# Kernel optimization log

Measured on AMD Instinct MI355X. Metric: run time of the kernel, lower is better.

The kernel has to match this reference:

```python
import jax, jax.numpy as jnp
from jax import lax
import numpy as np

NUM_HEAD = 4
D_MODEL = 160
HEAD_DIM = D_MODEL // NUM_HEAD  # 40
FEAT_DIM = 64
F_SIZE = (128, 128)
B = 4
LN_EPS = 1e-5
LEAKY_SLOPE = 0.01
DN = ('NCHW', 'OIHW', 'NCHW')


def setup_inputs() -> dict:
    key = jax.random.key(0)
    ks = jax.random.split(key, 10)
    pe_len = (F_SIZE[0] // 2) * (F_SIZE[1] // 2) + 1  # 4097
    s = 0.05
    return {
        'x': jax.random.normal(ks[0], (B, FEAT_DIM, F_SIZE[0], F_SIZE[1]), jnp.float32),
        'conv1_w': jax.random.normal(ks[1], (FEAT_DIM, FEAT_DIM, 2, 2), jnp.float32) * s,
        'conv1_b': jax.random.normal(ks[2], (FEAT_DIM,), jnp.float32) * s,
        'conv2_w': jax.random.normal(ks[3], (D_MODEL, FEAT_DIM, 1, 1), jnp.float32) * s,
        'conv2_b': jax.random.normal(ks[4], (D_MODEL,), jnp.float32) * s,
        'pe': jax.random.uniform(ks[5], (pe_len, 1), jnp.float32),
        'wq': jax.random.normal(ks[6], (D_MODEL, D_MODEL), jnp.float32) * s,
        'wk': jax.random.normal(ks[7], (D_MODEL, D_MODEL), jnp.float32) * s,
        'wv': jax.random.normal(ks[8], (D_MODEL, D_MODEL), jnp.float32) * s,
        'ln_w': jnp.ones((D_MODEL,), jnp.float32),
        'ln_b': jnp.zeros((D_MODEL,), jnp.float32),
    }


def reference(x, conv1_w, conv1_b, conv2_w, conv2_b, pe, wq, wk, wv, ln_w, ln_b):
    b = x.shape[0]
    # patch embed: stride-2 conv -> 1x1 conv -> LeakyReLU
    f = lax.conv_general_dilated(x, conv1_w, (2, 2), 'VALID', dimension_numbers=DN)
    f = f + conv1_b[None, :, None, None]
    f = lax.conv_general_dilated(f, conv2_w, (1, 1), 'VALID', dimension_numbers=DN)
    f = f + conv2_b[None, :, None, None]
    f = jnp.where(f >= 0, f, LEAKY_SLOPE * f)
    _, c, h, w = f.shape  # [b, 160, 64, 64]
    f = f.reshape(b, c, h * w).transpose(0, 2, 1)  # [b, s, d]
    # pad one extra token at end of sequence, add positional encoding [s+1, 1]
    f = jnp.pad(f, ((0, 0), (0, 1), (0, 0))) + pe  # [b, s+1, d]
    s1 = f.shape[1]
    # torch Linear (no bias): y = x @ W.T
    q = (f @ wq.T).reshape(b, s1, NUM_HEAD, HEAD_DIM).transpose(0, 2, 1, 3)
    k = (f @ wk.T).reshape(b, s1, NUM_HEAD, HEAD_DIM).transpose(0, 2, 1, 3)
    v = (f @ wv.T).reshape(b, s1, NUM_HEAD, HEAD_DIM).transpose(0, 2, 1, 3)
    score = jnp.einsum('bhqd,bhkd->bhqk', q, k) / jnp.sqrt(jnp.float32(HEAD_DIM))
    score = jax.nn.softmax(score, axis=-1)
    att = jnp.einsum('bhqk,bhkd->bhqd', score, v)  # [b, h, s+1, hd]
    cat = att.transpose(0, 2, 1, 3).reshape(b, s1, D_MODEL)
    feat = cat[:, :-1, :]  # drop padded token -> [b, s, d]
    # residual LayerNorm: LN(feat) + feat
    mu = jnp.mean(feat, axis=-1, keepdims=True)
    var = jnp.mean(jnp.square(feat - mu), axis=-1, keepdims=True)
    ln = (feat - mu) / jnp.sqrt(var + LN_EPS) * ln_w + ln_b
    feat = ln + feat
    feat = feat.transpose(0, 2, 1).reshape(b, D_MODEL, h, w)  # [b, 160, 64, 64]
    feat = jnp.repeat(jnp.repeat(feat, 2, axis=2), 2, axis=3)
    return feat
```

## Files before the change

kernel.cpp:

```cpp
#include <hip/hip_runtime.h>

typedef _Float16 f16;
typedef _Float16 half2v __attribute__((ext_vector_type(2)));
typedef _Float16 half4v __attribute__((ext_vector_type(4)));
typedef _Float16 half8 __attribute__((ext_vector_type(8)));
typedef float f32x4 __attribute__((ext_vector_type(4)));
typedef unsigned u32x4 __attribute__((ext_vector_type(4)));

#define MFMA16(a, b, c) __builtin_amdgcn_mfma_f32_16x16x32_f16((a), (b), (c), 0, 0, 0)

__device__ __forceinline__ unsigned pk2(float a, float b) {
  return __builtin_bit_cast(unsigned, __builtin_amdgcn_cvt_pkrtz(a, b));
}

__device__ __forceinline__ void plswap_pair(unsigned& a, unsigned& b) {
  asm("s_nop 1\n\t"
      "v_permlane32_swap_b32 %0, %1\n\t"
      "v_permlane16_swap_b32 %0, %1"
      : "+v"(a), "+v"(b));
}


__global__ __launch_bounds__(256) void k_prep(
    const float* __restrict__ wq, const float* __restrict__ wk,
    const float* __restrict__ wv, f16* __restrict__ wf) {
  int kind = blockIdx.y;
  const float* src = (kind == 0) ? wq : (kind == 1 ? wk : wv);
  int i4 = blockIdx.x * 256 + threadIdx.x;
  f32x4 v = *(const f32x4*)(src + i4 * 4);
  uint2 u = {pk2(v[0], v[1]), pk2(v[2], v[3])};
  *(uint2*)(wf + (size_t)kind * 25600 + i4 * 4) = u;
}

__global__ __launch_bounds__(256) void k_conv(
    const float* __restrict__ x, const float* __restrict__ w1, const float* __restrict__ b1,
    const float* __restrict__ w2, const float* __restrict__ b2, const float* __restrict__ pe,
    const float* __restrict__ wq, const float* __restrict__ wk, const float* __restrict__ wv,
    f16* __restrict__ fh, f16* __restrict__ q_h, f16* __restrict__ k_h,
    f16* __restrict__ vt_h, float* __restrict__ kmaxp) {
  __shared__ __attribute__((aligned(16))) char smem[112192];
  f16* fT   = (f16*)smem;
  f16* xh   = (f16*)(smem + 21504);
  f16* w1h  = (f16*)(smem + 55360);
  f16* c1t  = (f16*)(smem + 55360);
  float* red160 = (float*)(smem + 64576);
  f16* w2h  = (f16*)(smem + 89152);

  const float c1l = 0.15811388300841898f * 1.4426950408889634f;

  int y = blockIdx.x, b = blockIdx.y;
  int t = threadIdx.x, lane = t & 63, wv4 = t >> 6, quad = lane >> 4, col = lane & 15;
  int s0 = y * 64;

  const float* xb = x + (b * 64) * 16384 + (2 * y) * 128;
#pragma unroll
  for (int it = 0; it < 32; ++it) {
    int flat = t + it * 256;
    int pos = flat & 63, r = (flat >> 6) & 1, ci = flat >> 7;
    float2 v = *(const float2*)(xb + ci * 16384 + r * 128 + 2 * pos);
    *(unsigned*)(xh + pos * 264 + ci * 4 + r * 2) = pk2(v.x, v.y);
  }
#pragma unroll
  for (int it = 0; it < 16; ++it) {
    int i4 = t + it * 256;
    int co = i4 >> 6, q4 = (i4 & 63) * 4;
    f32x4 v = *(const f32x4*)(w1 + co * 256 + q4);
    uint2 u = {pk2(v[0], v[1]), pk2(v[2], v[3])};
    *(uint2*)(w1h + co * 264 + q4) = u;
  }
#pragma unroll
  for (int it = 0; it < 10; ++it) {
    int i4 = t + it * 256;
    int c2 = i4 >> 4, q4 = (i4 & 15) * 4;
    f32x4 v = *(const f32x4*)(w2 + c2 * 64 + q4);
    uint2 u = {pk2(v[0], v[1]), pk2(v[2], v[3])};
    *(uint2*)(w2h + c2 * 72 + q4) = u;
  }
  __syncthreads();

  float b1v[4];
#pragma unroll
  for (int r = 0; r < 4; ++r) b1v[r] = b1[wv4 * 16 + quad * 4 + r];
  f32x4 acc1[4];
#pragma unroll
  for (int nt = 0; nt < 4; ++nt)
#pragma unroll
    for (int r = 0; r < 4; ++r) acc1[nt][r] = b1v[r];
#pragma unroll
  for (int kk = 0; kk < 8; ++kk) {
    half8 a = *(half8*)(w1h + (wv4 * 16 + col) * 264 + kk * 32 + quad * 8);
#pragma unroll
    for (int nt = 0; nt < 4; ++nt) {
      half8 bfr = *(half8*)(xh + (nt * 16 + col) * 264 + kk * 32 + quad * 8);
      acc1[nt] = MFMA16(a, bfr, acc1[nt]);
    }
  }
  __syncthreads();
#pragma unroll
  for (int nt = 0; nt < 4; ++nt) {
    uint2 u = {pk2(acc1[nt][0], acc1[nt][1]), pk2(acc1[nt][2], acc1[nt][3])};
    *(uint2*)(c1t + (nt * 16 + col) * 72 + wv4 * 16 + quad * 4) = u;
  }
  __syncthreads();

  f32x4 acc2[10];
#pragma unroll
  for (int mt = 0; mt < 10; ++mt)
#pragma unroll
    for (int r = 0; r < 4; ++r) acc2[mt][r] = b2[mt * 16 + quad * 4 + r];
  half8 bb0 = *(half8*)(c1t + (wv4 * 16 + col) * 72 + quad * 8);
  half8 bb1 = *(half8*)(c1t + (wv4 * 16 + col) * 72 + 32 + quad * 8);
#pragma unroll
  for (int mt = 0; mt < 10; ++mt) {
    half8 a0 = *(half8*)(w2h + (mt * 16 + col) * 72 + quad * 8);
    half8 a1 = *(half8*)(w2h + (mt * 16 + col) * 72 + 32 + quad * 8);
    acc2[mt] = MFMA16(a0, bb0, acc2[mt]);
    acc2[mt] = MFMA16(a1, bb1, acc2[mt]);
  }
  float pes = pe[s0 + wv4 * 16 + col];
#pragma unroll
  for (int mt = 0; mt < 10; ++mt) {
    float p[4];
#pragma unroll
    for (int r = 0; r < 4; ++r) {
      float v = acc2[mt][r];
      v = (v >= 0.f) ? v : 0.01f * v;
      p[r] = v + pes;
    }
    uint2 u = {pk2(p[0], p[1]), pk2(p[2], p[3])};
    *(uint2*)(fT + (wv4 * 16 + col) * 168 + mt * 16 + quad * 4) = u;
  }
  __syncthreads();

#pragma unroll
  for (int it = 0; it < 5; ++it) {
    int flat = t + it * 256;
    int row = flat / 20, seg = flat - row * 20;
    *(uint4*)(fh + ((size_t)b * 4096 + s0 + row) * 160 + seg * 8) =
        *(const uint4*)(fT + row * 168 + seg * 8);
  }

  if (y == 63) {
    float pe4 = pe[4096];
    if (t < 160) {
      int hh = t / 40, d = t - hh * 40, bh = b * 4 + hh;
#pragma unroll
      for (int kind = 0; kind < 3; ++kind) {
        const float* wsp = (kind == 0) ? wq : (kind == 1 ? wk : wv);
        const float* wr = wsp + t * 160;
        float rs = 0.f;
#pragma unroll
        for (int c4 = 0; c4 < 40; ++c4) {
          f32x4 v = *(const f32x4*)(wr + c4 * 4);
          rs += v[0] + v[1] + v[2] + v[3];
        }
        float val = pe4 * rs;
        if (kind == 0)      q_h[((size_t)bh * 4097 + 4096) * 40 + d] = (f16)(val * c1l);
        else if (kind == 1) { k_h[((size_t)bh * 4160 + 4096) * 40 + d] = (f16)val;
                              red160[t] = val * val; }
        else                vt_h[((size_t)bh * 40 + d) * 4160 + 4096] = (f16)val;
      }
    }
    __syncthreads();
    if (t < 4) {
      float s = 0.f;
#pragma unroll
      for (int j = 0; j < 40; ++j) s += red160[t * 40 + j];
      kmaxp[(b * 4 + t) * 65 + 64] = s;
    }
  }
}

__global__ __launch_bounds__(256) void k_qkv(
    const f16* __restrict__ fh, const f16* __restrict__ wf,
    f16* __restrict__ q_h, f16* __restrict__ k_h, f16* __restrict__ vt_h) {
  __shared__ __attribute__((aligned(16))) f16 Lv[160 * 72];
  int y = blockIdx.x, b = blockIdx.y, kind = blockIdx.z;
  int t = threadIdx.x, lane = t & 63, wvv = t >> 6, quad = lane >> 4, col = lane & 15;
  int s0 = y * 64;
  const float c1l = 0.15811388300841898f * 1.4426950408889634f;
  const f16* wk_ = wf + (size_t)kind * 25600;

  half8 af[5];
  int rowA = wvv * 16 + col;
#pragma unroll
  for (int kk = 0; kk < 5; ++kk)
    af[kk] = *(const half8*)(fh + ((size_t)b * 4096 + s0 + rowA) * 160 + kk * 32 + quad * 8);

#pragma unroll
  for (int n0 = 0; n0 < 10; ++n0) {
    f32x4 acc; acc[0] = 0.f; acc[1] = 0.f; acc[2] = 0.f; acc[3] = 0.f;
    int rowB = n0 * 16 + col;
#pragma unroll
    for (int kk = 0; kk < 5; ++kk) {
      half8 bf = *(const half8*)(wk_ + rowB * 160 + kk * 32 + quad * 8);
      acc = MFMA16(af[kk], bf, acc);
    }
    int o = n0 * 16 + col;
    int hh = o / 40, d = o - hh * 40;
    int bh = b * 4 + hh;
    if (kind == 2) {
      half4v hv;
#pragma unroll
      for (int r = 0; r < 4; ++r) hv[r] = (f16)acc[r];
      *(half4v*)(Lv + o * 72 + wvv * 16 + quad * 4) = hv;
    } else {
#pragma unroll
      for (int r = 0; r < 4; ++r) {
        int s = s0 + wvv * 16 + quad * 4 + r;
        if (kind == 0) q_h[((size_t)bh * 4097 + s) * 40 + d] = (f16)(acc[r] * c1l);
        else           k_h[((size_t)bh * 4160 + s) * 40 + d] = (f16)acc[r];
      }
    }
  }
  if (kind == 2) {
    __syncthreads();
#pragma unroll
    for (int it = 0; it < 5; ++it) {
      int c = t + it * 256;
      int row = c >> 3, seg = c & 7;
      int hh = row / 40, d = row - hh * 40;
      *(uint4*)(vt_h + ((size_t)(b * 4 + hh) * 40 + d) * 4160 + s0 + seg * 8) =
          *(const uint4*)(Lv + row * 72 + seg * 8);
    }
  }
}

__global__ __launch_bounds__(256) void k_sq(
    const f16* __restrict__ k_h, float* __restrict__ kmaxp) {
  int t = threadIdx.x, lane = t & 63, wvv = t >> 6;
  int slot = blockIdx.x * 4 + wvv;
  int bh = blockIdx.y;
  int s = slot * 64 + lane;
  const f16* kr = k_h + ((size_t)bh * 4160 + s) * 40;
  float sum = 0.f;
#pragma unroll
  for (int i = 0; i < 5; ++i) {
    half8 v = *(const half8*)(kr + i * 8);
#pragma unroll
    for (int j = 0; j < 8; ++j) { float xv = (float)v[j]; sum += xv * xv; }
  }
#pragma unroll
  for (int d = 1; d < 64; d <<= 1) sum = fmaxf(sum, __shfl_xor(sum, d));
  if (lane == 0) kmaxp[bh * 65 + slot] = sum;
}

__global__ __launch_bounds__(256, 4) void k_attn(
    const f16* __restrict__ q_h, const f16* __restrict__ k_h,
    const f16* __restrict__ vt_h, const float* __restrict__ kmaxp,
    float* __restrict__ pacc) {
  __shared__ __attribute__((aligned(16))) f16 Ks[2][64 * 40];
  __shared__ __attribute__((aligned(16))) f16 Vs[2][40 * 72];
  __shared__ __attribute__((aligned(16))) f16 Ones[8];
  __shared__ __attribute__((aligned(16))) f16 Zro[8];
  __shared__ __attribute__((aligned(16))) float red4[4];

  int qt = blockIdx.x, bh = blockIdx.y, ks = blockIdx.z;
  int qbase = qt * 128;
  int t = threadIdx.x, lane = t & 63, wv = t >> 6, quad = lane >> 4, col = lane & 15;
  int gbase = ks * 33;
  int nIter = 33 - ks;

  if (t < 8) { Zro[t] = (f16)0; Ones[t] = (f16)1; }
  {
    float vm = (t < 65) ? kmaxp[bh * 65 + t] : 0.f;
#pragma unroll
    for (int d = 1; d < 64; d <<= 1) vm = fmaxf(vm, __shfl_xor(vm, d));
    if (lane == 0) red4[wv] = vm;
  }

  const f16* khb = k_h + ((size_t)bh * 4160 + gbase * 64) * 40;
  const f16* vtb = vt_h + (size_t)bh * 40 * 4160;
  int vrow = t >> 3, vseg = t & 7;
  uint4 rka = *(const uint4*)(khb + t * 8);
  uint4 rkb = {0, 0, 0, 0}, rvb = {0, 0, 0, 0};
  if (t < 64) rkb = *(const uint4*)(khb + (256 + t) * 8);
  uint4 rva = *(const uint4*)(vtb + vrow * 4160 + gbase * 64 + vseg * 8);
  if (t < 64) rvb = *(const uint4*)(vtb + (32 + vrow) * 4160 + gbase * 64 + vseg * 8);

  half8 zero8;
#pragma unroll
  for (int j = 0; j < 8; ++j) zero8[j] = (f16)0;

  half8 bq[2][2], q32[2];
#pragma unroll
  for (int nt = 0; nt < 2; ++nt) {
    const f16* qr = q_h + ((size_t)bh * 4097 + qbase + wv * 32 + nt * 16 + col) * 40;
    bq[nt][0] = *(const half8*)(qr + quad * 8);
    q32[nt] = *(const half8*)(qr + 32);
  }
  __syncthreads();

  float mk = fmaxf(fmaxf(red4[0], red4[1]), fmaxf(red4[2], red4[3]));

#pragma unroll
  for (int nt = 0; nt < 2; ++nt) {
    float s = 0.f;
#pragma unroll
    for (int j = 0; j < 8; ++j) {
      float a0 = (float)bq[nt][0][j];
      s += a0 * a0;
    }
    s += __shfl_xor(s, 16);
    s += __shfl_xor(s, 32);
#pragma unroll
    for (int j = 0; j < 8; ++j) {
      float a1 = (float)q32[nt][j];
      s += a1 * a1;
    }
    float mfl = sqrtf(s * mk) - 14.0f;
    half8 e = zero8;
    e[0] = (f16)(-mfl);
    bq[nt][1] = (quad == 0) ? q32[nt] : ((quad == 1) ? e : zero8);
  }

  f32x4 o_[2][3];
#pragma unroll
  for (int a = 0; a < 2; ++a)
#pragma unroll
    for (int b2 = 0; b2 < 3; ++b2)
#pragma unroll
      for (int r = 0; r < 4; ++r) o_[a][b2][r] = 0.f;

  for (int kt = 0; kt < nIter; ++kt) {
    int bsel = kt & 1;
    int g = gbase + kt;
    *(uint4*)(&Ks[bsel][t * 8]) = rka;
    if (t < 64) *(uint4*)(&Ks[bsel][(256 + t) * 8]) = rkb;
    *(uint4*)(&Vs[bsel][vrow * 72 + vseg * 8]) = rva;
    if (t < 64) *(uint4*)(&Vs[bsel][(32 + vrow) * 72 + vseg * 8]) = rvb;
    if (kt + 1 < nIter) {
      const f16* kn = khb + (size_t)(kt + 1) * 2560;
      int k0n = (g + 1) << 6;
      rka = *(const uint4*)(kn + t * 8);
      if (t < 64) rkb = *(const uint4*)(kn + (256 + t) * 8);
      rva = *(const uint4*)(vtb + vrow * 4160 + k0n + vseg * 8);
      if (t < 64) rvb = *(const uint4*)(vtb + (32 + vrow) * 4160 + k0n + vseg * 8);
    }
    __syncthreads();

    bool lastt = (g == 64);

    f32x4 acc[4][2];
#pragma unroll
    for (int mt = 0; mt < 4; ++mt) {
      int row = mt * 16 + col;
      half8 ak0 = *(half8*)(&Ks[bsel][row * 40 + quad * 8]);
      const f16* pa1 = (quad == 0) ? &Ks[bsel][row * 40 + 32]
                                   : ((quad == 1) ? Ones : Zro);
      half8 ak1 = *(half8*)pa1;
#pragma unroll
      for (int nt = 0; nt < 2; ++nt) {
        f32x4 a; a[0] = 0.f; a[1] = 0.f; a[2] = 0.f; a[3] = 0.f;
        a = MFMA16(ak0, bq[nt][0], a);
        a = MFMA16(ak1, bq[nt][1], a);
        acc[mt][nt] = a;
      }
    }

    half8 pa[2][2];
#pragma unroll
    for (int kk2 = 0; kk2 < 2; ++kk2)
#pragma unroll
      for (int nt = 0; nt < 2; ++nt) {
        float p0[4], p1[4];
#pragma unroll
        for (int r = 0; r < 4; ++r) {
          p0[r] = __builtin_amdgcn_exp2f(acc[kk2 * 2][nt][r]);
          p1[r] = __builtin_amdgcn_exp2f(acc[kk2 * 2 + 1][nt][r]);
        }
        if (__builtin_expect(lastt, 0)) {
#pragma unroll
          for (int r = 0; r < 4; ++r) {
            p0[r] = (kk2 == 0 && (quad * 4 + r) == 0) ? p0[r] : 0.f;
            p1[r] = 0.f;
          }
        }
        unsigned sr[4];
        sr[0] = pk2(p0[0], p0[1]);
        sr[1] = pk2(p0[2], p0[3]);
        sr[2] = pk2(p1[0], p1[1]);
        sr[3] = pk2(p1[2], p1[3]);
        plswap_pair(sr[0], sr[2]);
        plswap_pair(sr[1], sr[3]);
        u32x4 uu; uu[0] = sr[0]; uu[1] = sr[1]; uu[2] = sr[2]; uu[3] = sr[3];
        pa[kk2][nt] = __builtin_bit_cast(half8, uu);
      }

#pragma unroll
    for (int kk2 = 0; kk2 < 2; ++kk2)
#pragma unroll
      for (int nv = 0; nv < 3; ++nv) {
        int d = nv * 16 + col;
        const f16* vp = (d < 40) ? &Vs[bsel][d * 72 + kk2 * 32 + quad * 8]
                                 : ((d == 40) ? Ones : Zro);
        half8 bv = *(half8*)vp;
        o_[0][nv] = MFMA16(pa[kk2][0], bv, o_[0][nv]);
        o_[1][nv] = MFMA16(pa[kk2][1], bv, o_[1][nv]);
      }
  }

  float* pb = pacc + (size_t)(ks * 16 + bh) * 4096 * 48;
#pragma unroll
  for (int mtq = 0; mtq < 2; ++mtq)
#pragma unroll
    for (int nv = 0; nv < 3; ++nv)
#pragma unroll
      for (int r = 0; r < 4; ++r) {
        int q = qbase + wv * 32 + mtq * 16 + quad * 4 + r;
        pb[(size_t)q * 48 + nv * 16 + col] = o_[mtq][nv][r];
      }
}

__global__ __launch_bounds__(256) void k_ln_out(
    const float* __restrict__ pacc, const float* __restrict__ lnw,
    const float* __restrict__ lnb, float* __restrict__ out) {
  __shared__ float g[16 * 164];
  __shared__ float linv[16 * 4];
  int y = blockIdx.x, b = blockIdx.y, z = blockIdx.z, t = threadIdx.x;
  const size_t P1 = (size_t)16 * 4096 * 48;
  int w0 = z * 16;
  if (t < 64) {
    int row = t >> 2, h = t & 3;
    size_t i0 = ((size_t)(b * 4 + h) * 4096 + y * 64 + w0 + row) * 48 + 40;
    linv[row * 4 + h] = 1.f / (pacc[i0] + pacc[P1 + i0]);
  }
  __syncthreads();
#pragma unroll
  for (int it = 0; it < 3; ++it) {
    int flat = t + it * 256;
    if (flat < 640) {
      int row = flat / 40, dq = flat - row * 40;
      int h = dq / 10, d = (dq - h * 10) * 4;
      size_t idx = ((size_t)(b * 4 + h) * 4096 + y * 64 + w0 + row) * 48 + d;
      f32x4 v0 = *(const f32x4*)(pacc + idx);
      f32x4 v1 = *(const f32x4*)(pacc + P1 + idx);
      float li = linv[row * 4 + h];
      f32x4 gv;
#pragma unroll
      for (int j = 0; j < 4; ++j) gv[j] = (v0[j] + v1[j]) * li;
      *(f32x4*)(g + row * 164 + h * 40 + d) = gv;
    }
  }
  __syncthreads();
  int row = t >> 4, part = t & 15;
  float* gr = g + row * 164 + part * 10;
  float s1 = 0.f, s2 = 0.f;
#pragma unroll
  for (int j = 0; j < 10; ++j) { float v = gr[j]; s1 += v; s2 += v * v; }
  s1 += __shfl_xor(s1, 1); s1 += __shfl_xor(s1, 2);
  s1 += __shfl_xor(s1, 4); s1 += __shfl_xor(s1, 8);
  s2 += __shfl_xor(s2, 1); s2 += __shfl_xor(s2, 2);
  s2 += __shfl_xor(s2, 4); s2 += __shfl_xor(s2, 8);
  float mu = s1 * (1.f / 160.f);
  float var = s2 * (1.f / 160.f) - mu * mu;
  float inv = rsqrtf(var + 1e-5f);
  const float* lw = lnw + part * 10;
  const float* lb = lnb + part * 10;
#pragma unroll
  for (int j = 0; j < 10; ++j) {
    float v = gr[j];
    gr[j] = (v - mu) * inv * lw[j] + lb[j] + v;
  }
  __syncthreads();
  int Yo = t >> 7, rem = t & 127, xp = rem & 31, cpar = rem >> 5;
  int rl = xp >> 1;
  float* ob = out + (2 * y + Yo) * 128 + z * 32 + xp;
  for (int c = cpar; c < 160; c += 4)
    ob[(size_t)(b * 160 + c) * 16384] = g[rl * 164 + c];
}

extern "C" void kernel_launch(void* const* d_in, const int* in_sizes, int n_in,
                              void* d_out, int out_size, void* d_ws, size_t ws_size,
                              hipStream_t stream) {
  const float* x   = (const float*)d_in[0];
  const float* w1  = (const float*)d_in[1];
  const float* b1  = (const float*)d_in[2];
  const float* w2  = (const float*)d_in[3];
  const float* b2  = (const float*)d_in[4];
  const float* pe  = (const float*)d_in[5];
  const float* wq  = (const float*)d_in[6];
  const float* wk  = (const float*)d_in[7];
  const float* wvp = (const float*)d_in[8];
  const float* lnw = (const float*)d_in[9];
  const float* lnb = (const float*)d_in[10];
  float* out = (float*)d_out;

  char* p = (char*)d_ws;
  f16* q_h   = (f16*)p;   p += (size_t)16 * 4097 * 40 * 2;
  f16* k_h   = (f16*)p;   p += (size_t)16 * 4160 * 40 * 2;
  f16* vt_h  = (f16*)p;   p += (size_t)16 * 40 * 4160 * 2;
  float* pacc = (float*)p; p += (size_t)2 * 16 * 4096 * 48 * 4;
  float* kmaxp = (float*)p; p += 16 * 65 * 4;
  f16* fh    = (f16*)p;   p += (size_t)4 * 4096 * 160 * 2;
  f16* wf    = (f16*)p;   p += (size_t)3 * 160 * 160 * 2;

  k_prep<<<dim3(25, 3), 256, 0, stream>>>(wq, wk, wvp, wf);
  k_conv<<<dim3(64, 4), 256, 0, stream>>>(x, w1, b1, w2, b2, pe, wq, wk, wvp,
                                          fh, q_h, k_h, vt_h, kmaxp);
  k_qkv<<<dim3(64, 4, 3), 256, 0, stream>>>(fh, wf, q_h, k_h, vt_h);
  k_sq<<<dim3(16, 16), 256, 0, stream>>>(k_h, kmaxp);
  k_attn<<<dim3(32, 16, 2), 256, 0, stream>>>(q_h, k_h, vt_h, kmaxp, pacc);
  k_ln_out<<<dim3(64, 4, 4), 256, 0, stream>>>(pacc, lnw, lnb, out);
}
```

Measured before the change: 201.5 us.

## Split attention block into 8 waves with 16 queries each

After: 211.3 us. +4.8%, slower.

```diff
diff --git a/kernel.cpp b/kernel.cpp
--- a/kernel.cpp
+++ b/kernel.cpp
@@ -245,7 +245,7 @@
   if (lane == 0) kmaxp[bh * 65 + slot] = sum;
 }
 
-__global__ __launch_bounds__(256, 4) void k_attn(
+__global__ __launch_bounds__(512, 6) void k_attn(
     const f16* __restrict__ q_h, const f16* __restrict__ k_h,
     const f16* __restrict__ vt_h, const float* __restrict__ kmaxp,
     float* __restrict__ pacc) {
@@ -253,11 +253,11 @@
   __shared__ __attribute__((aligned(16))) f16 Vs[2][40 * 72];
   __shared__ __attribute__((aligned(16))) f16 Ones[8];
   __shared__ __attribute__((aligned(16))) f16 Zro[8];
-  __shared__ __attribute__((aligned(16))) float red4[4];
+  __shared__ __attribute__((aligned(16))) float red8[8];
 
   int qt = blockIdx.x, bh = blockIdx.y, ks = blockIdx.z;
   int qbase = qt * 128;
-  int t = threadIdx.x, lane = t & 63, wv = t >> 6, quad = lane >> 4, col = lane & 15;
+  int t = threadIdx.x, lane = t & 63, wid = t >> 6, quad = lane >> 4, col = lane & 15;
   int gbase = ks * 33;
   int nIter = 33 - ks;
 
@@ -266,82 +266,100 @@
     float vm = (t < 65) ? kmaxp[bh * 65 + t] : 0.f;
 #pragma unroll
     for (int d = 1; d < 64; d <<= 1) vm = fmaxf(vm, __shfl_xor(vm, d));
-    if (lane == 0) red4[wv] = vm;
+    if (lane == 0) red8[wid] = vm;
   }
 
   const f16* khb = k_h + ((size_t)bh * 4160 + gbase * 64) * 40;
   const f16* vtb = vt_h + (size_t)bh * 40 * 4160;
-  int vrow = t >> 3, vseg = t & 7;
-  uint4 rka = *(const uint4*)(khb + t * 8);
-  uint4 rkb = {0, 0, 0, 0}, rvb = {0, 0, 0, 0};
-  if (t < 64) rkb = *(const uint4*)(khb + (256 + t) * 8);
-  uint4 rva = *(const uint4*)(vtb + vrow * 4160 + gbase * 64 + vseg * 8);
-  if (t < 64) rvb = *(const uint4*)(vtb + (32 + vrow) * 4160 + gbase * 64 + vseg * 8);
+
+  uint4 r0, r1 = {0, 0, 0, 0};
+  {
+    int k00 = gbase << 6;
+    if (t < 320) {
+      r0 = *(const uint4*)(khb + t * 8);
+    } else {
+      int j = t - 320;
+      r0 = *(const uint4*)(vtb + (size_t)(j >> 3) * 4160 + k00 + (j & 7) * 8);
+    }
+    if (t < 128) {
+      int j = 192 + t;
+      r1 = *(const uint4*)(vtb + (size_t)(j >> 3) * 4160 + k00 + (j & 7) * 8);
+    }
+  }
 
   half8 zero8;
 #pragma unroll
   for (int j = 0; j < 8; ++j) zero8[j] = (f16)0;
 
-  half8 bq[2][2], q32[2];
-#pragma unroll
-  for (int nt = 0; nt < 2; ++nt) {
-    const f16* qr = q_h + ((size_t)bh * 4097 + qbase + wv * 32 + nt * 16 + col) * 40;
-    bq[nt][0] = *(const half8*)(qr + quad * 8);
-    q32[nt] = *(const half8*)(qr + 32);
-  }
-  __syncthreads();
-
-  float mk = fmaxf(fmaxf(red4[0], red4[1]), fmaxf(red4[2], red4[3]));
-
-#pragma unroll
-  for (int nt = 0; nt < 2; ++nt) {
+  half8 bq0, bq1, q32v;
+  {
+    const f16* qr = q_h + ((size_t)bh * 4097 + qbase + wid * 16 + col) * 40;
+    bq0 = *(const half8*)(qr + quad * 8);
+    q32v = *(const half8*)(qr + 32);
+  }
+  __syncthreads();
+
+  float mk = fmaxf(fmaxf(fmaxf(red8[0], red8[1]), fmaxf(red8[2], red8[3])),
+                   fmaxf(fmaxf(red8[4], red8[5]), fmaxf(red8[6], red8[7])));
+
+  {
     float s = 0.f;
 #pragma unroll
     for (int j = 0; j < 8; ++j) {
-      float a0 = (float)bq[nt][0][j];
+      float a0 = (float)bq0[j];
       s += a0 * a0;
     }
     s += __shfl_xor(s, 16);
     s += __shfl_xor(s, 32);
 #pragma unroll
     for (int j = 0; j < 8; ++j) {
-      float a1 = (float)q32[nt][j];
+      float a1 = (float)q32v[j];
       s += a1 * a1;
     }
     float mfl = sqrtf(s * mk) - 14.0f;
     half8 e = zero8;
     e[0] = (f16)(-mfl);
-    bq[nt][1] = (quad == 0) ? q32[nt] : ((quad == 1) ? e : zero8);
-  }
-
-  f32x4 o_[2][3];
-#pragma unroll
-  for (int a = 0; a < 2; ++a)
-#pragma unroll
-    for (int b2 = 0; b2 < 3; ++b2)
-#pragma unroll
-      for (int r = 0; r < 4; ++r) o_[a][b2][r] = 0.f;
+    bq1 = (quad == 0) ? q32v : ((quad == 1) ? e : zero8);
+  }
+
+  f32x4 o_[3];
+#pragma unroll
+  for (int nv = 0; nv < 3; ++nv)
+#pragma unroll
+    for (int r = 0; r < 4; ++r) o_[nv][r] = 0.f;
 
   for (int kt = 0; kt < nIter; ++kt) {
     int bsel = kt & 1;
     int g = gbase + kt;
-    *(uint4*)(&Ks[bsel][t * 8]) = rka;
-    if (t < 64) *(uint4*)(&Ks[bsel][(256 + t) * 8]) = rkb;
-    *(uint4*)(&Vs[bsel][vrow * 72 + vseg * 8]) = rva;
-    if (t < 64) *(uint4*)(&Vs[bsel][(32 + vrow) * 72 + vseg * 8]) = rvb;
+    if (t < 320) {
+      *(uint4*)(&Ks[bsel][t * 8]) = r0;
+    } else {
+      int j = t - 320;
+      *(uint4*)(&Vs[bsel][(j >> 3) * 72 + (j & 7) * 8]) = r0;
+    }
+    if (t < 128) {
+      int j = 192 + t;
+      *(uint4*)(&Vs[bsel][(j >> 3) * 72 + (j & 7) * 8]) = r1;
+    }
     if (kt + 1 < nIter) {
       const f16* kn = khb + (size_t)(kt + 1) * 2560;
       int k0n = (g + 1) << 6;
-      rka = *(const uint4*)(kn + t * 8);
-      if (t < 64) rkb = *(const uint4*)(kn + (256 + t) * 8);
-      rva = *(const uint4*)(vtb + vrow * 4160 + k0n + vseg * 8);
-      if (t < 64) rvb = *(const uint4*)(vtb + (32 + vrow) * 4160 + k0n + vseg * 8);
+      if (t < 320) {
+        r0 = *(const uint4*)(kn + t * 8);
+      } else {
+        int j = t - 320;
+        r0 = *(const uint4*)(vtb + (size_t)(j >> 3) * 4160 + k0n + (j & 7) * 8);
+      }
+      if (t < 128) {
+        int j = 192 + t;
+        r1 = *(const uint4*)(vtb + (size_t)(j >> 3) * 4160 + k0n + (j & 7) * 8);
+      }
     }
     __syncthreads();
 
     bool lastt = (g == 64);
 
-    f32x4 acc[4][2];
+    f32x4 acc[4];
 #pragma unroll
     for (int mt = 0; mt < 4; ++mt) {
       int row = mt * 16 + col;
@@ -349,43 +367,38 @@
       const f16* pa1 = (quad == 0) ? &Ks[bsel][row * 40 + 32]
                                    : ((quad == 1) ? Ones : Zro);
       half8 ak1 = *(half8*)pa1;
-#pragma unroll
-      for (int nt = 0; nt < 2; ++nt) {
-        f32x4 a; a[0] = 0.f; a[1] = 0.f; a[2] = 0.f; a[3] = 0.f;
-        a = MFMA16(ak0, bq[nt][0], a);
-        a = MFMA16(ak1, bq[nt][1], a);
-        acc[mt][nt] = a;
-      }
-    }
-
-    half8 pa[2][2];
-#pragma unroll
-    for (int kk2 = 0; kk2 < 2; ++kk2)
-#pragma unroll
-      for (int nt = 0; nt < 2; ++nt) {
-        float p0[4], p1[4];
+      f32x4 a; a[0] = 0.f; a[1] = 0.f; a[2] = 0.f; a[3] = 0.f;
+      a = MFMA16(ak0, bq0, a);
+      a = MFMA16(ak1, bq1, a);
+      acc[mt] = a;
+    }
+
+    half8 pa[2];
+#pragma unroll
+    for (int kk2 = 0; kk2 < 2; ++kk2) {
+      float p0[4], p1[4];
+#pragma unroll
+      for (int r = 0; r < 4; ++r) {
+        p0[r] = __builtin_amdgcn_exp2f(acc[kk2 * 2][r]);
+        p1[r] = __builtin_amdgcn_exp2f(acc[kk2 * 2 + 1][r]);
+      }
+      if (__builtin_expect(lastt, 0)) {
 #pragma unroll
         for (int r = 0; r < 4; ++r) {
-          p0[r] = __builtin_amdgcn_exp2f(acc[kk2 * 2][nt][r]);
-          p1[r] = __builtin_amdgcn_exp2f(acc[kk2 * 2 + 1][nt][r]);
+          p0[r] = (kk2 == 0 && (quad * 4 + r) == 0) ? p0[r] : 0.f;
+          p1[r] = 0.f;
         }
-        if (__builtin_expect(lastt, 0)) {
-#pragma unroll
-          for (int r = 0; r < 4; ++r) {
-            p0[r] = (kk2 == 0 && (quad * 4 + r) == 0) ? p0[r] : 0.f;
-            p1[r] = 0.f;
-          }
-        }
-        unsigned sr[4];
-        sr[0] = pk2(p0[0], p0[1]);
-        sr[1] = pk2(p0[2], p0[3]);
-        sr[2] = pk2(p1[0], p1[1]);
-        sr[3] = pk2(p1[2], p1[3]);
-        plswap_pair(sr[0], sr[2]);
-        plswap_pair(sr[1], sr[3]);
-        u32x4 uu; uu[0] = sr[0]; uu[1] = sr[1]; uu[2] = sr[2]; uu[3] = sr[3];
-        pa[kk2][nt] = __builtin_bit_cast(half8, uu);
-      }
+      }
+      unsigned sr[4];
+      sr[0] = pk2(p0[0], p0[1]);
+      sr[1] = pk2(p0[2], p0[3]);
+      sr[2] = pk2(p1[0], p1[1]);
+      sr[3] = pk2(p1[2], p1[3]);
+      plswap_pair(sr[0], sr[2]);
+      plswap_pair(sr[1], sr[3]);
+      u32x4 uu; uu[0] = sr[0]; uu[1] = sr[1]; uu[2] = sr[2]; uu[3] = sr[3];
+      pa[kk2] = __builtin_bit_cast(half8, uu);
+    }
 
 #pragma unroll
     for (int kk2 = 0; kk2 < 2; ++kk2)
@@ -395,21 +408,18 @@
         const f16* vp = (d < 40) ? &Vs[bsel][d * 72 + kk2 * 32 + quad * 8]
                                  : ((d == 40) ? Ones : Zro);
         half8 bv = *(half8*)vp;
-        o_[0][nv] = MFMA16(pa[kk2][0], bv, o_[0][nv]);
-        o_[1][nv] = MFMA16(pa[kk2][1], bv, o_[1][nv]);
+        o_[nv] = MFMA16(pa[kk2], bv, o_[nv]);
       }
   }
 
   float* pb = pacc + (size_t)(ks * 16 + bh) * 4096 * 48;
 #pragma unroll
-  for (int mtq = 0; mtq < 2; ++mtq)
-#pragma unroll
-    for (int nv = 0; nv < 3; ++nv)
-#pragma unroll
-      for (int r = 0; r < 4; ++r) {
-        int q = qbase + wv * 32 + mtq * 16 + quad * 4 + r;
-        pb[(size_t)q * 48 + nv * 16 + col] = o_[mtq][nv][r];
-      }
+  for (int nv = 0; nv < 3; ++nv)
+#pragma unroll
+    for (int r = 0; r < 4; ++r) {
+      int q = qbase + wid * 16 + quad * 4 + r;
+      pb[(size_t)q * 48 + nv * 16 + col] = o_[nv][r];
+    }
 }
 
 __global__ __launch_bounds__(256) void k_ln_out(
@@ -500,6 +510,6 @@
                                           fh, q_h, k_h, vt_h, kmaxp);
   k_qkv<<<dim3(64, 4, 3), 256, 0, stream>>>(fh, wf, q_h, k_h, vt_h);
   k_sq<<<dim3(16, 16), 256, 0, stream>>>(k_h, kmaxp);
-  k_attn<<<dim3(32, 16, 2), 256, 0, stream>>>(q_h, k_h, vt_h, kmaxp, pacc);
+  k_attn<<<dim3(32, 16, 2), 512, 0, stream>>>(q_h, k_h, vt_h, kmaxp, pacc);
   k_ln_out<<<dim3(64, 4, 4), 256, 0, stream>>>(pacc, lnw, lnb, out);
 }
```

## Precompute conv weights in fp16 and split conv kernel into half-row tiles

Applied to the files above, without the earlier changes.

New measurement: 209.6 us. 1.04x slower.

```diff
diff --git a/kernel.cpp b/kernel.cpp
--- a/kernel.cpp
+++ b/kernel.cpp
@@ -23,103 +23,93 @@
 
 __global__ __launch_bounds__(256) void k_prep(
     const float* __restrict__ wq, const float* __restrict__ wk,
-    const float* __restrict__ wv, f16* __restrict__ wf) {
-  int kind = blockIdx.y;
-  const float* src = (kind == 0) ? wq : (kind == 1 ? wk : wv);
+    const float* __restrict__ wv, const float* __restrict__ w1,
+    const float* __restrict__ w2, f16* __restrict__ wf) {
   int i4 = blockIdx.x * 256 + threadIdx.x;
-  f32x4 v = *(const f32x4*)(src + i4 * 4);
+  const float* src;
+  int idx;
+  if (i4 < 19200) { src = (i4 < 6400) ? wq : (i4 < 12800 ? wk : wv); idx = i4 % 6400; }
+  else if (i4 < 23296) { src = w1; idx = i4 - 19200; }
+  else { src = w2; idx = i4 - 23296; }
+  f32x4 v = *(const f32x4*)(src + idx * 4);
   uint2 u = {pk2(v[0], v[1]), pk2(v[2], v[3])};
-  *(uint2*)(wf + (size_t)kind * 25600 + i4 * 4) = u;
+  *(uint2*)(wf + i4 * 4) = u;
 }
 
 __global__ __launch_bounds__(256) void k_conv(
-    const float* __restrict__ x, const float* __restrict__ w1, const float* __restrict__ b1,
-    const float* __restrict__ w2, const float* __restrict__ b2, const float* __restrict__ pe,
+    const float* __restrict__ x, const f16* __restrict__ wf,
+    const float* __restrict__ b1, const float* __restrict__ b2,
+    const float* __restrict__ pe,
     const float* __restrict__ wq, const float* __restrict__ wk, const float* __restrict__ wv,
     f16* __restrict__ fh, f16* __restrict__ q_h, f16* __restrict__ k_h,
     f16* __restrict__ vt_h, float* __restrict__ kmaxp) {
-  __shared__ __attribute__((aligned(16))) char smem[112192];
-  f16* fT   = (f16*)smem;
-  f16* xh   = (f16*)(smem + 21504);
-  f16* w1h  = (f16*)(smem + 55360);
-  f16* c1t  = (f16*)(smem + 55360);
-  float* red160 = (float*)(smem + 64576);
-  f16* w2h  = (f16*)(smem + 89152);
-
+  __shared__ __attribute__((aligned(16))) char smem[32896];
+  f16* xh   = (f16*)smem;
+  f16* fT   = (f16*)(smem + 16896);
+  f16* c1t  = (f16*)(smem + 27648);
+  float* red160 = (float*)(smem + 32256);
+
+  const f16* w1f = wf + 76800;
+  const f16* w2f = wf + 93184;
   const float c1l = 0.15811388300841898f * 1.4426950408889634f;
 
-  int y = blockIdx.x, b = blockIdx.y;
+  int yt = blockIdx.x, b = blockIdx.y;
+  int i = yt >> 1, j0 = (yt & 1) * 32;
+  int pbase = i * 64 + j0;
   int t = threadIdx.x, lane = t & 63, wv4 = t >> 6, quad = lane >> 4, col = lane & 15;
-  int s0 = y * 64;
-
-  const float* xb = x + (b * 64) * 16384 + (2 * y) * 128;
-#pragma unroll
-  for (int it = 0; it < 32; ++it) {
+
+#pragma unroll
+  for (int it = 0; it < 16; ++it) {
     int flat = t + it * 256;
-    int pos = flat & 63, r = (flat >> 6) & 1, ci = flat >> 7;
-    float2 v = *(const float2*)(xb + ci * 16384 + r * 128 + 2 * pos);
+    int pos = flat & 31, r = (flat >> 5) & 1, ci = flat >> 6;
+    float2 v = *(const float2*)(x + (size_t)(b * 64 + ci) * 16384 +
+                                (2 * i + r) * 128 + 2 * (j0 + pos));
     *(unsigned*)(xh + pos * 264 + ci * 4 + r * 2) = pk2(v.x, v.y);
   }
-#pragma unroll
-  for (int it = 0; it < 16; ++it) {
-    int i4 = t + it * 256;
-    int co = i4 >> 6, q4 = (i4 & 63) * 4;
-    f32x4 v = *(const f32x4*)(w1 + co * 256 + q4);
-    uint2 u = {pk2(v[0], v[1]), pk2(v[2], v[3])};
-    *(uint2*)(w1h + co * 264 + q4) = u;
-  }
-#pragma unroll
-  for (int it = 0; it < 10; ++it) {
-    int i4 = t + it * 256;
-    int c2 = i4 >> 4, q4 = (i4 & 15) * 4;
-    f32x4 v = *(const f32x4*)(w2 + c2 * 64 + q4);
-    uint2 u = {pk2(v[0], v[1]), pk2(v[2], v[3])};
-    *(uint2*)(w2h + c2 * 72 + q4) = u;
-  }
   __syncthreads();
 
   float b1v[4];
 #pragma unroll
   for (int r = 0; r < 4; ++r) b1v[r] = b1[wv4 * 16 + quad * 4 + r];
-  f32x4 acc1[4];
-#pragma unroll
-  for (int nt = 0; nt < 4; ++nt)
+  f32x4 acc1[2];
+#pragma unroll
+  for (int nt = 0; nt < 2; ++nt)
 #pragma unroll
     for (int r = 0; r < 4; ++r) acc1[nt][r] = b1v[r];
 #pragma unroll
   for (int kk = 0; kk < 8; ++kk) {
-    half8 a = *(half8*)(w1h + (wv4 * 16 + col) * 264 + kk * 32 + quad * 8);
-#pragma unroll
-    for (int nt = 0; nt < 4; ++nt) {
+    half8 a = *(const half8*)(w1f + (wv4 * 16 + col) * 256 + kk * 32 + quad * 8);
+#pragma unroll
+    for (int nt = 0; nt < 2; ++nt) {
       half8 bfr = *(half8*)(xh + (nt * 16 + col) * 264 + kk * 32 + quad * 8);
       acc1[nt] = MFMA16(a, bfr, acc1[nt]);
     }
   }
-  __syncthreads();
-#pragma unroll
-  for (int nt = 0; nt < 4; ++nt) {
+#pragma unroll
+  for (int nt = 0; nt < 2; ++nt) {
     uint2 u = {pk2(acc1[nt][0], acc1[nt][1]), pk2(acc1[nt][2], acc1[nt][3])};
     *(uint2*)(c1t + (nt * 16 + col) * 72 + wv4 * 16 + quad * 4) = u;
   }
   __syncthreads();
 
-  f32x4 acc2[10];
-#pragma unroll
-  for (int mt = 0; mt < 10; ++mt)
-#pragma unroll
-    for (int r = 0; r < 4; ++r) acc2[mt][r] = b2[mt * 16 + quad * 4 + r];
-  half8 bb0 = *(half8*)(c1t + (wv4 * 16 + col) * 72 + quad * 8);
-  half8 bb1 = *(half8*)(c1t + (wv4 * 16 + col) * 72 + 32 + quad * 8);
-#pragma unroll
-  for (int mt = 0; mt < 10; ++mt) {
-    half8 a0 = *(half8*)(w2h + (mt * 16 + col) * 72 + quad * 8);
-    half8 a1 = *(half8*)(w2h + (mt * 16 + col) * 72 + 32 + quad * 8);
+  int pg = wv4 & 1, ch = wv4 >> 1;
+  f32x4 acc2[5];
+#pragma unroll
+  for (int mt = 0; mt < 5; ++mt)
+#pragma unroll
+    for (int r = 0; r < 4; ++r) acc2[mt][r] = b2[ch * 80 + mt * 16 + quad * 4 + r];
+  half8 bb0 = *(half8*)(c1t + (pg * 16 + col) * 72 + quad * 8);
+  half8 bb1 = *(half8*)(c1t + (pg * 16 + col) * 72 + 32 + quad * 8);
+#pragma unroll
+  for (int mt = 0; mt < 5; ++mt) {
+    half8 a0 = *(const half8*)(w2f + (ch * 80 + mt * 16 + col) * 64 + quad * 8);
+    half8 a1 = *(const half8*)(w2f + (ch * 80 + mt * 16 + col) * 64 + 32 + quad * 8);
     acc2[mt] = MFMA16(a0, bb0, acc2[mt]);
     acc2[mt] = MFMA16(a1, bb1, acc2[mt]);
   }
-  float pes = pe[s0 + wv4 * 16 + col];
-#pragma unroll
-  for (int mt = 0; mt < 10; ++mt) {
+  float pes = pe[pbase + pg * 16 + col];
+#pragma unroll
+  for (int mt = 0; mt < 5; ++mt) {
     float p[4];
 #pragma unroll
     for (int r = 0; r < 4; ++r) {
@@ -128,19 +118,21 @@
       p[r] = v + pes;
     }
     uint2 u = {pk2(p[0], p[1]), pk2(p[2], p[3])};
-    *(uint2*)(fT + (wv4 * 16 + col) * 168 + mt * 16 + quad * 4) = u;
-  }
-  __syncthreads();
-
-#pragma unroll
-  for (int it = 0; it < 5; ++it) {
+    *(uint2*)(fT + (pg * 16 + col) * 168 + ch * 80 + mt * 16 + quad * 4) = u;
+  }
+  __syncthreads();
+
+#pragma unroll
+  for (int it = 0; it < 3; ++it) {
     int flat = t + it * 256;
-    int row = flat / 20, seg = flat - row * 20;
-    *(uint4*)(fh + ((size_t)b * 4096 + s0 + row) * 160 + seg * 8) =
-        *(const uint4*)(fT + row * 168 + seg * 8);
-  }
-
-  if (y == 63) {
+    if (flat < 640) {
+      int row = flat / 20, seg = flat - row * 20;
+      *(uint4*)(fh + ((size_t)b * 4096 + pbase + row) * 160 + seg * 8) =
+          *(const uint4*)(fT + row * 168 + seg * 8);
+    }
+  }
+
+  if (yt == 127) {
     float pe4 = pe[4096];
     if (t < 160) {
       int hh = t / 40, d = t - hh * 40, bh = b * 4 + hh;
@@ -493,11 +485,11 @@
   float* pacc = (float*)p; p += (size_t)2 * 16 * 4096 * 48 * 4;
   float* kmaxp = (float*)p; p += 16 * 65 * 4;
   f16* fh    = (f16*)p;   p += (size_t)4 * 4096 * 160 * 2;
-  f16* wf    = (f16*)p;   p += (size_t)3 * 160 * 160 * 2;
-
-  k_prep<<<dim3(25, 3), 256, 0, stream>>>(wq, wk, wvp, wf);
-  k_conv<<<dim3(64, 4), 256, 0, stream>>>(x, w1, b1, w2, b2, pe, wq, wk, wvp,
-                                          fh, q_h, k_h, vt_h, kmaxp);
+  f16* wf    = (f16*)p;   p += (size_t)103424 * 2;
+
+  k_prep<<<dim3(101), 256, 0, stream>>>(wq, wk, wvp, w1, w2, wf);
+  k_conv<<<dim3(128, 4), 256, 0, stream>>>(x, wf, b1, b2, pe, wq, wk, wvp,
+                                           fh, q_h, k_h, vt_h, kmaxp);
   k_qkv<<<dim3(64, 4, 3), 256, 0, stream>>>(fh, wf, q_h, k_h, vt_h);
   k_sq<<<dim3(16, 16), 256, 0, stream>>>(k_h, kmaxp);
   k_attn<<<dim3(32, 16, 2), 256, 0, stream>>>(q_h, k_h, vt_h, kmaxp, pacc);
```
